# Kernel tuning notes

Hardware: AMD Instinct MI355X
Metric: run time of the kernel (lower is better)

Reference implementation:

```python
import jax, jax.numpy as jnp
import numpy as np

N = 8192
E = 262144

def gcn_conv(x, W, b, row, col, w):
    # PyG GCNConv with self-loops already appended to (row, col, w).
    h = x @ W                                   # [N, out]
    deg = jax.ops.segment_sum(w, col, num_segments=N)
    dinv = jnp.where(deg > 0, jax.lax.rsqrt(deg), 0.0)
    norm = dinv[row] * w * dinv[col]            # [E+N]
    out = jax.ops.segment_sum(norm[:, None] * h[row], col, num_segments=N)
    return out + b

def setup_inputs() -> dict:
    key = jax.random.key(0)
    ks = jax.random.split(key, 10)
    return {
        "x": jax.random.normal(ks[0], (N, 512), jnp.float32),
        "edge_index": jax.random.randint(ks[1], (2, E), 0, N, jnp.int64),
        "edge_weight": jax.random.uniform(ks[2], (E,), jnp.float32),
        "noise": jax.random.normal(ks[3], (N, 64), jnp.float32),
        "W1": jax.random.normal(ks[4], (512, 256), jnp.float32) * 0.05,
        "b1": jnp.zeros((256,), jnp.float32),
        "W2": jax.random.normal(ks[5], (256, 256), jnp.float32) * 0.05,
        "b2": jnp.zeros((256,), jnp.float32),
        "Wm": jax.random.normal(ks[6], (256, 64), jnp.float32) * 0.05,
        "bm": jnp.zeros((64,), jnp.float32),
        "Ws": jax.random.normal(ks[7], (256, 64), jnp.float32) * 0.05,
        "bs": jnp.zeros((64,), jnp.float32),
    }

def reference(x, edge_index, edge_weight, noise, W1, b1, W2, b2, Wm, bm, Ws, bs):
    # add self-loops once (weight 1.0), shared by all GCN layers
    loop = jnp.arange(N, dtype=edge_index.dtype)
    row = jnp.concatenate([edge_index[0], loop])
    col = jnp.concatenate([edge_index[1], loop])
    w = jnp.concatenate([edge_weight, jnp.ones((N,), edge_weight.dtype)])

    h = jax.nn.relu(gcn_conv(x, W1, b1, row, col, w))
    h = jax.nn.relu(gcn_conv(h, W2, b2, row, col, w))
    mean = jax.nn.relu(gcn_conv(h, Wm, bm, row, col, w))
    log_std = jax.nn.relu(gcn_conv(h, Ws, bs, row, col, w))
    z = noise * jnp.exp(log_std) + mean          # [N, 64]
    adj = jax.nn.sigmoid(z @ z.T)                # [N, N]
    return jnp.triu(adj, k=1)
```

## Files before the change

### kernel.cpp

```cpp
#include <hip/hip_runtime.h>
#include <hip/hip_bf16.h>

#define NN 8192
#define NE 262144

typedef __attribute__((ext_vector_type(8))) short bf16x8;
typedef __attribute__((ext_vector_type(4))) float f32x4;

__global__ __launch_bounds__(256) void k_init(float* __restrict__ deg, int* __restrict__ counts,
                                              int* __restrict__ cnt2) {
  int i = blockIdx.x * 256 + threadIdx.x;
  if (i < NN) { deg[i] = 1.0f; counts[i] = 0; cnt2[i] = 0; }
}

__global__ __launch_bounds__(256) void k_count(const int* __restrict__ ei, const float* __restrict__ w,
                                               float* __restrict__ deg, int* __restrict__ counts) {
  int e = blockIdx.x * 256 + threadIdx.x;
  if (e < NE) {
    int c = ei[NE + e];
    atomicAdd(&deg[c], w[e]);
    atomicAdd(&counts[c], 1);
  }
}

__global__ __launch_bounds__(1024) void k_scan(const int* __restrict__ counts, int* __restrict__ offs) {
  __shared__ int part[1024];
  int t = threadIdx.x;
  int base = t * 8;
  int local[8];
  int s = 0;
#pragma unroll
  for (int j = 0; j < 8; ++j) { local[j] = counts[base + j]; s += local[j]; }
  part[t] = s;
  __syncthreads();
  for (int off = 1; off < 1024; off <<= 1) {
    int v = (t >= off) ? part[t - off] : 0;
    __syncthreads();
    part[t] += v;
    __syncthreads();
  }
  int run = (t > 0) ? part[t - 1] : 0;
#pragma unroll
  for (int j = 0; j < 8; ++j) { offs[base + j] = run; run += local[j]; }
  if (t == 1023) offs[NN] = run;
}

__global__ __launch_bounds__(256) void k_scatter(const int* __restrict__ ei, const float* __restrict__ w,
                                                 const float* __restrict__ deg, const int* __restrict__ offs,
                                                 int* __restrict__ cnt2, int* __restrict__ csr_row,
                                                 float* __restrict__ csr_val) {
  int e = blockIdx.x * 256 + threadIdx.x;
  if (e < NE) {
    int r = ei[e], c = ei[NE + e];
    int slot = offs[c] + atomicAdd(&cnt2[c], 1);
    csr_row[slot] = r;
    csr_val[slot] = rsqrtf(deg[r]) * w[e] * rsqrtf(deg[c]);
  }
}

__global__ __launch_bounds__(256) void k_splitX(const float* __restrict__ x,
                                                __hip_bfloat16* __restrict__ xh,
                                                __hip_bfloat16* __restrict__ xl) {
  size_t i = ((size_t)blockIdx.x * 256 + threadIdx.x) * 4;
  f32x4 v = *(const f32x4*)(x + i);
#pragma unroll
  for (int j = 0; j < 4; ++j) {
    __hip_bfloat16 h = __float2bfloat16(v[j]);
    xh[i + j] = h;
    xl[i + j] = __float2bfloat16(v[j] - __bfloat162float(h));
  }
}

__global__ __launch_bounds__(256) void k_splitW(const float* __restrict__ W,
                                                __hip_bfloat16* __restrict__ WhT,
                                                __hip_bfloat16* __restrict__ WlT, int K, int Nc) {
  int idx = blockIdx.x * 256 + threadIdx.x;
  if (idx < K * Nc) {
    int k = idx / Nc, n = idx - k * Nc;
    float v = W[idx];
    __hip_bfloat16 h = __float2bfloat16(v);
    WhT[(size_t)n * K + k] = h;
    WlT[(size_t)n * K + k] = __float2bfloat16(v - __bfloat162float(h));
  }
}

__global__ __launch_bounds__(256) void k_splitWcat(const float* __restrict__ Wm, const float* __restrict__ Wsw,
                                                   const float* __restrict__ bm, const float* __restrict__ bsv,
                                                   __hip_bfloat16* __restrict__ WhT,
                                                   __hip_bfloat16* __restrict__ WlT,
                                                   float* __restrict__ bcat) {
  int idx = blockIdx.x * 256 + threadIdx.x;
  int n = idx >> 8, k = idx & 255;
  float v = (n < 64) ? Wm[k * 64 + n] : Wsw[k * 64 + (n - 64)];
  __hip_bfloat16 h = __float2bfloat16(v);
  WhT[idx] = h;
  WlT[idx] = __float2bfloat16(v - __bfloat162float(h));
  if (blockIdx.x == 0 && threadIdx.x < 128)
    bcat[threadIdx.x] = (threadIdx.x < 64) ? bm[threadIdx.x] : bsv[threadIdx.x - 64];
}

__global__ __launch_bounds__(256) void k_gemm_mfma(const short* __restrict__ Ah, const short* __restrict__ Al,
                                                   const short* __restrict__ BhT, const short* __restrict__ BlT,
                                                   float* __restrict__ C, int K, int Nc) {
  int m0 = blockIdx.y * 64, n0 = blockIdx.x * 64;
  int wv = threadIdx.x >> 6, lane = threadIdx.x & 63;
  int wr = wv >> 1, wc = wv & 1;
  int lr = lane & 15, lk8 = (lane >> 4) << 3;
  int arow = m0 + wr * 32 + lr;
  int bcol = n0 + wc * 32 + lr;
  f32x4 acc[2][2] = {};
  for (int k0 = 0; k0 < K; k0 += 32) {
    bf16x8 ah[2], al[2], bh[2], bl[2];
#pragma unroll
    for (int rb = 0; rb < 2; ++rb) {
      size_t o = (size_t)(arow + rb * 16) * K + k0 + lk8;
      ah[rb] = *(const bf16x8*)(Ah + o);
      al[rb] = *(const bf16x8*)(Al + o);
    }
#pragma unroll
    for (int cb = 0; cb < 2; ++cb) {
      size_t o = (size_t)(bcol + cb * 16) * K + k0 + lk8;
      bh[cb] = *(const bf16x8*)(BhT + o);
      bl[cb] = *(const bf16x8*)(BlT + o);
    }
#pragma unroll
    for (int rb = 0; rb < 2; ++rb)
#pragma unroll
      for (int cb = 0; cb < 2; ++cb) {
        f32x4 c = acc[rb][cb];
        c = __builtin_amdgcn_mfma_f32_16x16x32_bf16(ah[rb], bh[cb], c, 0, 0, 0);
        c = __builtin_amdgcn_mfma_f32_16x16x32_bf16(ah[rb], bl[cb], c, 0, 0, 0);
        c = __builtin_amdgcn_mfma_f32_16x16x32_bf16(al[rb], bh[cb], c, 0, 0, 0);
        acc[rb][cb] = c;
      }
  }
  int orow = m0 + wr * 32 + ((lane >> 4) << 2);
  int ocol = n0 + wc * 32 + (lane & 15);
#pragma unroll
  for (int rb = 0; rb < 2; ++rb)
#pragma unroll
    for (int cb = 0; cb < 2; ++cb)
#pragma unroll
      for (int r = 0; r < 4; ++r)
        C[(size_t)(orow + rb * 16 + r) * Nc + ocol + cb * 16] = acc[rb][cb][r];
}

template <int D, bool SPLIT>
__global__ __launch_bounds__(256) void k_agg(const float* __restrict__ t, const float* __restrict__ deg,
                                             const int* __restrict__ csr_row, const float* __restrict__ csr_val,
                                             const int* __restrict__ offs, const float* __restrict__ bias,
                                             float* __restrict__ outf,
                                             __hip_bfloat16* __restrict__ outh,
                                             __hip_bfloat16* __restrict__ outl) {
  constexpr int V = D / 64;
  __shared__ int   srow[256];
  __shared__ float sval[256];
  __shared__ float sacc[4][D];
  int c = blockIdx.x;
  int tid = threadIdx.x;
  int w = tid >> 6, lane = tid & 63;
  int d0 = lane * V;
  float acc[V];
#pragma unroll
  for (int j = 0; j < V; ++j) acc[j] = 0.0f;
  int s0 = offs[c], s1 = offs[c + 1];
  for (int base = s0; base < s1; base += 256) {
    int cnt = s1 - base; if (cnt > 256) cnt = 256;
    __syncthreads();
    if (tid < cnt) { srow[tid] = csr_row[base + tid]; sval[tid] = csr_val[base + tid]; }
    __syncthreads();
    for (int s = w; s < cnt; s += 4) {
      int r = srow[s];
      float v = sval[s];
      const float* p = t + (size_t)r * D + d0;
      if constexpr (V == 4) {
        float4 pv = *(const float4*)p;
        acc[0] = fmaf(v, pv.x, acc[0]);
        acc[1] = fmaf(v, pv.y, acc[1]);
        acc[2] = fmaf(v, pv.z, acc[2]);
        acc[3] = fmaf(v, pv.w, acc[3]);
      } else {
        float2 pv = *(const float2*)p;
        acc[0] = fmaf(v, pv.x, acc[0]);
        acc[1] = fmaf(v, pv.y, acc[1]);
      }
    }
  }
#pragma unroll
  for (int j = 0; j < V; ++j) sacc[w][d0 + j] = acc[j];
  __syncthreads();
  if (tid < 64) {
    float di = rsqrtf(deg[c]);
    float selfw = di * di;
#pragma unroll
    for (int j = 0; j < V; ++j) {
      int d = tid * V + j;
      float a = sacc[0][d] + sacc[1][d] + sacc[2][d] + sacc[3][d];
      a = fmaf(selfw, t[(size_t)c * D + d], a);
      a = fmaxf(a + bias[d], 0.0f);
      if constexpr (SPLIT) {
        __hip_bfloat16 h = __float2bfloat16(a);
        outh[(size_t)c * D + d] = h;
        outl[(size_t)c * D + d] = __float2bfloat16(a - __bfloat162float(h));
      } else {
        outf[(size_t)c * D + d] = a;
      }
    }
  }
}

__global__ __launch_bounds__(256) void k_z(const float* __restrict__ gms, const float* __restrict__ noise,
                                           __hip_bfloat16* __restrict__ zh, __hip_bfloat16* __restrict__ zl) {
  int idx = blockIdx.x * 256 + threadIdx.x;
  int i = idx >> 6, k = idx & 63;
  float mean = gms[(size_t)i * 128 + k];
  float ls = gms[(size_t)i * 128 + 64 + k];
  float z = noise[idx] * __expf(ls) + mean;
  __hip_bfloat16 h = __float2bfloat16(z);
  zh[idx] = h;
  zl[idx] = __float2bfloat16(z - __bfloat162float(h));
}

__global__ __launch_bounds__(256) void k_final(const short* __restrict__ zh, const short* __restrict__ zl,
                                               float* __restrict__ out) {
  int ti = blockIdx.y, tj = blockIdx.x;
  int ri0 = ti * 128, cj0 = tj * 128;
  if (tj < ti) {
    f32x4 zz = {};
    int tr = threadIdx.x >> 5;
    int tc = (threadIdx.x & 31) << 2;
    float* base = out + (size_t)(ri0 + tr) * NN + cj0 + tc;
#pragma unroll
    for (int rr = 0; rr < 128; rr += 8)
      *(f32x4*)(base + (size_t)rr * NN) = zz;
    return;
  }
  int wv = threadIdx.x >> 6;
  int lane = threadIdx.x & 63;
  int wr = wv >> 1, wc = wv & 1;
  int lr = lane & 15;
  int lk = (lane >> 4) << 3;
  int arow = ri0 + wr * 64 + lr;
  int brow = cj0 + wc * 64 + lr;

  bf16x8 ah[4][2], al[4][2];
#pragma unroll
  for (int rb = 0; rb < 4; ++rb)
#pragma unroll
    for (int ks = 0; ks < 2; ++ks) {
      int o = (arow + rb * 16) * 64 + ks * 32 + lk;
      ah[rb][ks] = *(const bf16x8*)(zh + o);
      al[rb][ks] = *(const bf16x8*)(zl + o);
    }
  f32x4 acc[4][4] = {};
#pragma unroll
  for (int cb = 0; cb < 4; ++cb) {
    bf16x8 bh[2], bl[2];
#pragma unroll
    for (int ks = 0; ks < 2; ++ks) {
      int o = (brow + cb * 16) * 64 + ks * 32 + lk;
      bh[ks] = *(const bf16x8*)(zh + o);
      bl[ks] = *(const bf16x8*)(zl + o);
    }
#pragma unroll
    for (int rb = 0; rb < 4; ++rb) {
      f32x4 c = acc[rb][cb];
#pragma unroll
      for (int ks = 0; ks < 2; ++ks) {
        c = __builtin_amdgcn_mfma_f32_16x16x32_bf16(ah[rb][ks], bh[ks], c, 0, 0, 0);
        c = __builtin_amdgcn_mfma_f32_16x16x32_bf16(ah[rb][ks], bl[ks], c, 0, 0, 0);
        c = __builtin_amdgcn_mfma_f32_16x16x32_bf16(al[rb][ks], bh[ks], c, 0, 0, 0);
      }
      acc[rb][cb] = c;
    }
  }
  int orow = ri0 + wr * 64 + ((lane >> 4) << 2);
  int ocol = cj0 + wc * 64 + (lane & 15);
#pragma unroll
  for (int rb = 0; rb < 4; ++rb)
#pragma unroll
    for (int cb = 0; cb < 4; ++cb)
#pragma unroll
      for (int r = 0; r < 4; ++r) {
        int row = orow + rb * 16 + r;
        int col = ocol + cb * 16;
        float v = acc[rb][cb][r];
        float sg = 1.0f / (1.0f + __expf(-v));
        out[(size_t)row * NN + col] = (col > row) ? sg : 0.0f;
      }
}

extern "C" void kernel_launch(void* const* d_in, const int* in_sizes, int n_in,
                              void* d_out, int out_size, void* d_ws, size_t ws_size,
                              hipStream_t stream) {
  (void)in_sizes; (void)n_in; (void)out_size; (void)ws_size;
  const float* x     = (const float*)d_in[0];
  const int*   ei    = (const int*)d_in[1];
  const float* ew    = (const float*)d_in[2];
  const float* noise = (const float*)d_in[3];
  const float* W1    = (const float*)d_in[4];
  const float* b1    = (const float*)d_in[5];
  const float* W2    = (const float*)d_in[6];
  const float* b2    = (const float*)d_in[7];
  const float* Wm    = (const float*)d_in[8];
  const float* bm    = (const float*)d_in[9];
  const float* Wsw   = (const float*)d_in[10];
  const float* bsv   = (const float*)d_in[11];
  float* out = (float*)d_out;

  char* wsb = (char*)d_ws;
  size_t off = 0;
  auto bump = [&](size_t bytes) -> void* {
    void* p = wsb + off;
    off += (bytes + 255) & ~(size_t)255;
    return p;
  };
  float* deg     = (float*)bump((size_t)NN * 4);
  int*   counts  = (int*)bump((size_t)NN * 4);
  int*   offs    = (int*)bump((size_t)(NN + 1) * 4);
  int*   cnt2    = (int*)bump((size_t)NN * 4);
  int*   csr_row = (int*)bump((size_t)NE * 4);
  float* csr_val = (float*)bump((size_t)NE * 4);
  __hip_bfloat16* xh = (__hip_bfloat16*)bump((size_t)NN * 512 * 2);
  __hip_bfloat16* xl = (__hip_bfloat16*)bump((size_t)NN * 512 * 2);
  float* bufA    = (float*)bump((size_t)NN * 256 * 4);
  __hip_bfloat16* h1h = (__hip_bfloat16*)bump((size_t)NN * 256 * 2);
  __hip_bfloat16* h1l = (__hip_bfloat16*)bump((size_t)NN * 256 * 2);
  __hip_bfloat16* W1hT = (__hip_bfloat16*)bump((size_t)256 * 512 * 2);
  __hip_bfloat16* W1lT = (__hip_bfloat16*)bump((size_t)256 * 512 * 2);
  __hip_bfloat16* W2hT = (__hip_bfloat16*)bump((size_t)256 * 256 * 2);
  __hip_bfloat16* W2lT = (__hip_bfloat16*)bump((size_t)256 * 256 * 2);
  __hip_bfloat16* WchT = (__hip_bfloat16*)bump((size_t)128 * 256 * 2);
  __hip_bfloat16* WclT = (__hip_bfloat16*)bump((size_t)128 * 256 * 2);
  float* bcat    = (float*)bump((size_t)128 * 4);
  __hip_bfloat16* zh = (__hip_bfloat16*)bump((size_t)NN * 64 * 2);
  __hip_bfloat16* zl = (__hip_bfloat16*)bump((size_t)NN * 64 * 2);

  __hip_bfloat16* h2h = xh;
  __hip_bfloat16* h2l = xl;
  float* bufG = (float*)h1h;

  k_init<<<NN / 256, 256, 0, stream>>>(deg, counts, cnt2);
  k_count<<<NE / 256, 256, 0, stream>>>(ei, ew, deg, counts);
  k_scan<<<1, 1024, 0, stream>>>(counts, offs);
  k_scatter<<<NE / 256, 256, 0, stream>>>(ei, ew, deg, offs, cnt2, csr_row, csr_val);

  k_splitX<<<NN * 512 / 4 / 256, 256, 0, stream>>>(x, xh, xl);
  k_splitW<<<512, 256, 0, stream>>>(W1, W1hT, W1lT, 512, 256);
  k_splitW<<<256, 256, 0, stream>>>(W2, W2hT, W2lT, 256, 256);
  k_splitWcat<<<128, 256, 0, stream>>>(Wm, Wsw, bm, bsv, WchT, WclT, bcat);

  k_gemm_mfma<<<dim3(4, 128), 256, 0, stream>>>((const short*)xh, (const short*)xl,
                                                (const short*)W1hT, (const short*)W1lT, bufA, 512, 256);
  k_agg<256, true><<<NN, 256, 0, stream>>>(bufA, deg, csr_row, csr_val, offs, b1, nullptr, h1h, h1l);
  k_gemm_mfma<<<dim3(4, 128), 256, 0, stream>>>((const short*)h1h, (const short*)h1l,
                                                (const short*)W2hT, (const short*)W2lT, bufA, 256, 256);
  k_agg<256, true><<<NN, 256, 0, stream>>>(bufA, deg, csr_row, csr_val, offs, b2, nullptr, h2h, h2l);
  k_gemm_mfma<<<dim3(2, 128), 256, 0, stream>>>((const short*)h2h, (const short*)h2l,
                                                (const short*)WchT, (const short*)WclT, bufA, 256, 128);
  k_agg<128, false><<<NN, 256, 0, stream>>>(bufA, deg, csr_row, csr_val, offs, bcat, bufG, nullptr, nullptr);
  k_z<<<NN * 64 / 256, 256, 0, stream>>>(bufG, noise, zh, zl);
  k_final<<<dim3(64, 64), 256, 0, stream>>>((const short*)zh, (const short*)zl, out);
}
```

Measured before the change: 281.8 us.

## Split GCN aggregation into 64-column panels and stream final tile stores

The single aggregation kernel, which gathered all D features per edge, is replaced by several launches. Each launch handles one 64-column panel, so the gathered working set (8192 rows × 64 floats = 2 MB) can stay cache-resident across edges instead of spreading gathers over the full 8 MB feature matrix. The cost is re-reading the CSR structure once per panel, more kernel launches, and scalar instead of vector loads per lane. The final sigmoid GEMM kernel also now writes results after each column block, which shrinks live accumulator registers, and bufG gets its own buffer instead of aliasing h1h.

```diff
diff --git a/kernel.cpp b/kernel.cpp
--- a/kernel.cpp
+++ b/kernel.cpp
@@ -146,65 +146,43 @@
 }
 
 template <int D, bool SPLIT>
-__global__ __launch_bounds__(256) void k_agg(const float* __restrict__ t, const float* __restrict__ deg,
-                                             const int* __restrict__ csr_row, const float* __restrict__ csr_val,
-                                             const int* __restrict__ offs, const float* __restrict__ bias,
-                                             float* __restrict__ outf,
-                                             __hip_bfloat16* __restrict__ outh,
-                                             __hip_bfloat16* __restrict__ outl) {
-  constexpr int V = D / 64;
+__global__ __launch_bounds__(256) void k_aggp(const float* __restrict__ t, const float* __restrict__ deg,
+                                              const int* __restrict__ csr_row, const float* __restrict__ csr_val,
+                                              const int* __restrict__ offs, const float* __restrict__ bias,
+                                              float* __restrict__ outf,
+                                              __hip_bfloat16* __restrict__ outh,
+                                              __hip_bfloat16* __restrict__ outl,
+                                              int p0) {
   __shared__ int   srow[256];
   __shared__ float sval[256];
-  __shared__ float sacc[4][D];
+  __shared__ float sacc[4][64];
   int c = blockIdx.x;
   int tid = threadIdx.x;
   int w = tid >> 6, lane = tid & 63;
-  int d0 = lane * V;
-  float acc[V];
-#pragma unroll
-  for (int j = 0; j < V; ++j) acc[j] = 0.0f;
+  float acc = 0.0f;
   int s0 = offs[c], s1 = offs[c + 1];
   for (int base = s0; base < s1; base += 256) {
     int cnt = s1 - base; if (cnt > 256) cnt = 256;
     __syncthreads();
     if (tid < cnt) { srow[tid] = csr_row[base + tid]; sval[tid] = csr_val[base + tid]; }
     __syncthreads();
-    for (int s = w; s < cnt; s += 4) {
-      int r = srow[s];
-      float v = sval[s];
-      const float* p = t + (size_t)r * D + d0;
-      if constexpr (V == 4) {
-        float4 pv = *(const float4*)p;
-        acc[0] = fmaf(v, pv.x, acc[0]);
-        acc[1] = fmaf(v, pv.y, acc[1]);
-        acc[2] = fmaf(v, pv.z, acc[2]);
-        acc[3] = fmaf(v, pv.w, acc[3]);
-      } else {
-        float2 pv = *(const float2*)p;
-        acc[0] = fmaf(v, pv.x, acc[0]);
-        acc[1] = fmaf(v, pv.y, acc[1]);
-      }
-    }
-  }
-#pragma unroll
-  for (int j = 0; j < V; ++j) sacc[w][d0 + j] = acc[j];
+    for (int s = w; s < cnt; s += 4)
+      acc = fmaf(sval[s], t[(size_t)srow[s] * D + p0 + lane], acc);
+  }
+  sacc[w][lane] = acc;
   __syncthreads();
   if (tid < 64) {
+    int d = p0 + tid;
     float di = rsqrtf(deg[c]);
-    float selfw = di * di;
-#pragma unroll
-    for (int j = 0; j < V; ++j) {
-      int d = tid * V + j;
-      float a = sacc[0][d] + sacc[1][d] + sacc[2][d] + sacc[3][d];
-      a = fmaf(selfw, t[(size_t)c * D + d], a);
-      a = fmaxf(a + bias[d], 0.0f);
-      if constexpr (SPLIT) {
-        __hip_bfloat16 h = __float2bfloat16(a);
-        outh[(size_t)c * D + d] = h;
-        outl[(size_t)c * D + d] = __float2bfloat16(a - __bfloat162float(h));
-      } else {
-        outf[(size_t)c * D + d] = a;
-      }
+    float a = sacc[0][tid] + sacc[1][tid] + sacc[2][tid] + sacc[3][tid];
+    a = fmaf(di * di, t[(size_t)c * D + d], a);
+    a = fmaxf(a + bias[d], 0.0f);
+    if constexpr (SPLIT) {
+      __hip_bfloat16 h = __float2bfloat16(a);
+      outh[(size_t)c * D + d] = h;
+      outl[(size_t)c * D + d] = __float2bfloat16(a - __bfloat162float(h));
+    } else {
+      outf[(size_t)c * D + d] = a;
     }
   }
 }
@@ -252,7 +230,8 @@
       ah[rb][ks] = *(const bf16x8*)(zh + o);
       al[rb][ks] = *(const bf16x8*)(zl + o);
     }
-  f32x4 acc[4][4] = {};
+  int orow = ri0 + wr * 64 + ((lane >> 4) << 2);
+  int ocol = cj0 + wc * 64 + (lane & 15);
 #pragma unroll
   for (int cb = 0; cb < 4; ++cb) {
     bf16x8 bh[2], bl[2];
@@ -262,32 +241,29 @@
       bh[ks] = *(const bf16x8*)(zh + o);
       bl[ks] = *(const bf16x8*)(zl + o);
     }
+    f32x4 acc[4] = {};
 #pragma unroll
     for (int rb = 0; rb < 4; ++rb) {
-      f32x4 c = acc[rb][cb];
+      f32x4 c = acc[rb];
 #pragma unroll
       for (int ks = 0; ks < 2; ++ks) {
         c = __builtin_amdgcn_mfma_f32_16x16x32_bf16(ah[rb][ks], bh[ks], c, 0, 0, 0);
         c = __builtin_amdgcn_mfma_f32_16x16x32_bf16(ah[rb][ks], bl[ks], c, 0, 0, 0);
         c = __builtin_amdgcn_mfma_f32_16x16x32_bf16(al[rb][ks], bh[ks], c, 0, 0, 0);
       }
-      acc[rb][cb] = c;
-    }
-  }
-  int orow = ri0 + wr * 64 + ((lane >> 4) << 2);
-  int ocol = cj0 + wc * 64 + (lane & 15);
-#pragma unroll
-  for (int rb = 0; rb < 4; ++rb)
-#pragma unroll
-    for (int cb = 0; cb < 4; ++cb)
+      acc[rb] = c;
+    }
+#pragma unroll
+    for (int rb = 0; rb < 4; ++rb)
 #pragma unroll
       for (int r = 0; r < 4; ++r) {
         int row = orow + rb * 16 + r;
         int col = ocol + cb * 16;
-        float v = acc[rb][cb][r];
+        float v = acc[rb][r];
         float sg = 1.0f / (1.0f + __expf(-v));
         out[(size_t)row * NN + col] = (col > row) ? sg : 0.0f;
       }
+  }
 }
 
 extern "C" void kernel_launch(void* const* d_in, const int* in_sizes, int n_in,
@@ -335,10 +311,10 @@
   float* bcat    = (float*)bump((size_t)128 * 4);
   __hip_bfloat16* zh = (__hip_bfloat16*)bump((size_t)NN * 64 * 2);
   __hip_bfloat16* zl = (__hip_bfloat16*)bump((size_t)NN * 64 * 2);
+  float* bufG    = (float*)bump((size_t)NN * 128 * 4);
 
   __hip_bfloat16* h2h = xh;
   __hip_bfloat16* h2l = xl;
-  float* bufG = (float*)h1h;
 
   k_init<<<NN / 256, 256, 0, stream>>>(deg, counts, cnt2);
   k_count<<<NE / 256, 256, 0, stream>>>(ei, ew, deg, counts);
@@ -352,13 +328,16 @@
 
   k_gemm_mfma<<<dim3(4, 128), 256, 0, stream>>>((const short*)xh, (const short*)xl,
                                                 (const short*)W1hT, (const short*)W1lT, bufA, 512, 256);
-  k_agg<256, true><<<NN, 256, 0, stream>>>(bufA, deg, csr_row, csr_val, offs, b1, nullptr, h1h, h1l);
+  for (int p0 = 0; p0 < 256; p0 += 64)
+    k_aggp<256, true><<<NN, 256, 0, stream>>>(bufA, deg, csr_row, csr_val, offs, b1, nullptr, h1h, h1l, p0);
   k_gemm_mfma<<<dim3(4, 128), 256, 0, stream>>>((const short*)h1h, (const short*)h1l,
                                                 (const short*)W2hT, (const short*)W2lT, bufA, 256, 256);
-  k_agg<256, true><<<NN, 256, 0, stream>>>(bufA, deg, csr_row, csr_val, offs, b2, nullptr, h2h, h2l);
+  for (int p0 = 0; p0 < 256; p0 += 64)
+    k_aggp<256, true><<<NN, 256, 0, stream>>>(bufA, deg, csr_row, csr_val, offs, b2, nullptr, h2h, h2l, p0);
   k_gemm_mfma<<<dim3(2, 128), 256, 0, stream>>>((const short*)h2h, (const short*)h2l,
                                                 (const short*)WchT, (const short*)WclT, bufA, 256, 128);
-  k_agg<128, false><<<NN, 256, 0, stream>>>(bufA, deg, csr_row, csr_val, offs, bcat, bufG, nullptr, nullptr);
+  for (int p0 = 0; p0 < 128; p0 += 64)
+    k_aggp<128, false><<<NN, 256, 0, stream>>>(bufA, deg, csr_row, csr_val, offs, bcat, bufG, nullptr, nullptr, p0);
   k_z<<<NN * 64 / 256, 256, 0, stream>>>(bufG, noise, zh, zl);
   k_final<<<dim3(64, 64), 256, 0, stream>>>((const short*)zh, (const short*)zl, out);
 }
```

Result: slower. 369.6 us (+31.2%).
